# Kernel tuning notes

Measured on AMD Instinct MI355X. Metric: run time of the kernel, lower is better.

Reference implementation:

```python
import jax, jax.numpy as jnp
import numpy as np

B, T, C, H, E, TOPK, DR = 2, 2048, 768, 3072, 8, 2, 24


def setup_inputs() -> dict:
    key = jax.random.key(0)
    ks = jax.random.split(key, 16)
    std = 0.02
    n = lambda k, shape, s=std: (s * jax.random.normal(k, shape)).astype(jnp.float32)
    emb = jax.random.normal(ks[3], (E, DR), dtype=jnp.float32)
    emb = emb / (jnp.linalg.norm(emb, axis=-1, keepdims=True) + 1e-8)
    return {
        "x": jax.random.normal(ks[0], (B, T, C), dtype=jnp.float32),
        "router_w": n(ks[1], (E, C)),
        "probe_w": n(ks[2], (DR, C)),
        "router_emb": emb,
        "fatigue": jnp.zeros((E,), jnp.float32),
        "energy": jnp.ones((E,), jnp.float32),
        "w_fast1": n(ks[4], (E, C, H)),
        "w_slow1": n(ks[5], (E, C, H)),
        "h_fast1": n(ks[6], (E, C, H), 0.005),
        "m_gate1": jax.random.uniform(ks[7], (E,), dtype=jnp.float32),
        "b1": jnp.zeros((E, H), jnp.float32),
        "w_fast2": n(ks[8], (E, H, C)),
        "w_slow2": n(ks[9], (E, H, C)),
        "h_fast2": n(ks[10], (E, H, C), 0.005),
        "m_gate2": jax.random.uniform(ks[11], (E,), dtype=jnp.float32),
        "b2": jnp.zeros((E, C), jnp.float32),
    }


def _normalize(v, axis=-1, eps=1e-12):
    # matches F.normalize: v / max(||v||, eps)
    return v / jnp.maximum(jnp.linalg.norm(v, axis=axis, keepdims=True), eps)


def reference(x, router_w, probe_w, router_emb, fatigue, energy,
              w_fast1, w_slow1, h_fast1, m_gate1, b1,
              w_fast2, w_slow2, h_fast2, m_gate2, b2):
    Bd, Td, Cd = x.shape
    # --- router logits with biology-inspired biases ---
    logits = jnp.einsum('btc,ec->bte', x, router_w)            # nn.Linear, no bias
    tok_proxy = x.mean(axis=-1, keepdims=True)                  # [B,T,1]
    router_gain = jnp.linalg.norm(router_emb, axis=-1)          # [E]
    base_bias = 0.02 * tok_proxy                                # broadcasts over E
    gain_bias = 0.02 * tok_proxy * router_gain                  # [B,T,E]
    tok_unit = _normalize(jnp.einsum('btc,dc->btd', x, probe_w))
    align_bias = 0.02 * jnp.einsum('btd,ed->bte', tok_unit, _normalize(router_emb))
    logits = logits + base_bias + gain_bias + align_bias + 0.1 * energy - 0.1 * fatigue
    # --- top-k gating ---
    g, idx = jax.lax.top_k(logits, TOPK)                        # [B,T,K]
    gates = jax.nn.softmax(g, axis=-1)
    N = Bd * Td
    gates_full = jnp.zeros((N, E), x.dtype).at[
        jnp.arange(N)[:, None], idx.reshape(N, TOPK)].set(gates.reshape(N, TOPK))
    flat_x = x.reshape(N, Cd)
    # --- expert dispatch: dynamic W = w_fast + m_gate*w_slow + H_fast ---
    def body(acc, p):
        wf1, ws1, hf1, mg1, bb1, wf2, ws2, hf2, mg2, bb2, ge = p
        W1 = wf1 + mg1 * ws1 + hf1                              # [C,H]
        h = jnp.square(jnp.maximum(flat_x @ W1 + bb1, 0.0))     # relu(y)^2
        W2 = wf2 + mg2 * ws2 + hf2                              # [H,C]
        y = h @ W2 + bb2
        return acc + ge[:, None] * y, None
    out, _ = jax.lax.scan(
        body, jnp.zeros((N, Cd), x.dtype),
        (w_fast1, w_slow1, h_fast1, m_gate1, b1,
         w_fast2, w_slow2, h_fast2, m_gate2, b2, gates_full.T))
    return out.reshape(Bd, Td, Cd)
```

## Files before the change

kernel.cpp:

```cpp
#include <hip/hip_runtime.h>

typedef unsigned short u16;
typedef __attribute__((ext_vector_type(8))) short short8;
typedef __attribute__((ext_vector_type(8))) unsigned short ushort8;
typedef __attribute__((ext_vector_type(4))) unsigned short ushort4v;
typedef __attribute__((ext_vector_type(4))) float f32x4;

static constexpr int Cdim = 768;
static constexpr int Hdim = 3072;
static constexpr int Edim = 8;
static constexpr int Ntok = 4096;
static constexpr int DRc  = 24;
static constexpr int NSLOT = Ntok * 2;
static constexpr int NCHUNK = 8;
static constexpr int CCH = Cdim / NCHUNK;

static constexpr size_t OFF_XB   = 0;
static constexpr size_t OFF_W1T  = 6291456;
static constexpr size_t OFF_W2T  = 44040192;
static constexpr size_t OFF_HBUF = 81788928;
static constexpr size_t OFF_XT   = OFF_HBUF;
static constexpr size_t OFF_PART = OFF_HBUF + 12582912;
static constexpr size_t OFF_YB   = OFF_W1T;
static constexpr size_t OFF_TOK  = 132120576;
static constexpr size_t OFF_CNT  = 132382720;
static constexpr size_t OFF_OFFS = 132382752;
static constexpr size_t OFF_TSLOT= 132382784;
static constexpr size_t OFF_TG   = 132448320;

__device__ __forceinline__ u16 f2bf(float f) {
  unsigned u = __builtin_bit_cast(unsigned, f);
  u += 0x7fffu + ((u >> 16) & 1u);
  return (u16)(u >> 16);
}

__device__ __forceinline__ void gld16(const u16* g, u16* l) {
  __builtin_amdgcn_global_load_lds((const __attribute__((address_space(1))) unsigned int*)g,
                                   (__attribute__((address_space(3))) unsigned int*)l,
                                   16, 0, 0);
}

__global__ __launch_bounds__(256)
void prep_x2_kernel(const float* __restrict__ x, u16* __restrict__ x16,
                    float* __restrict__ xT) {
  __shared__ float tile[64][65];
  const int c0 = blockIdx.x * 64;
  const int t0 = blockIdx.y * 64;
  const int tid = threadIdx.x;
  const int row = tid >> 4, col = (tid & 15) * 4;
  #pragma unroll
  for (int i = 0; i < 4; i++) {
    int r = row + i * 16;
    size_t idx = (size_t)(t0 + r) * Cdim + c0 + col;
    float4 v = *(const float4*)(x + idx);
    tile[r][col + 0] = v.x; tile[r][col + 1] = v.y;
    tile[r][col + 2] = v.z; tile[r][col + 3] = v.w;
    ushort4v o = { f2bf(v.x), f2bf(v.y), f2bf(v.z), f2bf(v.w) };
    *reinterpret_cast<ushort4v*>(x16 + idx) = o;
  }
  __syncthreads();
  const int c = tid >> 2, tg = (tid & 3) * 16;
  #pragma unroll
  for (int q = 0; q < 4; q++) {
    float4 w;
    w.x = tile[tg + q * 4 + 0][c];
    w.y = tile[tg + q * 4 + 1][c];
    w.z = tile[tg + q * 4 + 2][c];
    w.w = tile[tg + q * 4 + 3][c];
    *reinterpret_cast<float4*>(xT + (size_t)(c0 + c) * Ntok + t0 + tg + q * 4) = w;
  }
}

__global__ __launch_bounds__(256)
void prep_wt_kernel(const float* __restrict__ wf, const float* __restrict__ wsl,
                    const float* __restrict__ hf, const float* __restrict__ mg,
                    u16* __restrict__ outw, const int R, const int Ccol) {
  __shared__ u16 tileT[64][66];
  const int e = blockIdx.z;
  const int r0 = blockIdx.x * 64, c0 = blockIdx.y * 64;
  const float m = mg[e];
  const size_t base = (size_t)e * R * Ccol;
  const int t = threadIdx.x;
  const int cr = t >> 4, cc = (t & 15) * 4;
  #pragma unroll
  for (int i = 0; i < 4; i++) {
    int r = cr + i * 16;
    size_t idx = base + (size_t)(r0 + r) * Ccol + (c0 + cc);
    float4 a = *(const float4*)(wf + idx);
    float4 b = *(const float4*)(wsl + idx);
    float4 h = *(const float4*)(hf + idx);
    tileT[cc + 0][r] = f2bf(fmaf(m, b.x, a.x) + h.x);
    tileT[cc + 1][r] = f2bf(fmaf(m, b.y, a.y) + h.y);
    tileT[cc + 2][r] = f2bf(fmaf(m, b.z, a.z) + h.z);
    tileT[cc + 3][r] = f2bf(fmaf(m, b.w, a.w) + h.w);
  }
  __syncthreads();
  const int oc = t >> 2, ch = (t & 3) * 16;
  ushort8 o0, o1;
  #pragma unroll
  for (int j = 0; j < 8; j++) { o0[j] = tileT[oc][ch + j]; o1[j] = tileT[oc][ch + 8 + j]; }
  size_t oidx = ((size_t)e * Ccol + c0 + oc) * R + r0 + ch;
  *reinterpret_cast<ushort8*>(outw + oidx) = o0;
  *reinterpret_cast<ushort8*>(outw + oidx + 8) = o1;
}

__global__ __launch_bounds__(256)
void logits_part_kernel(const float* __restrict__ xT, const float* __restrict__ router_w,
                        const float* __restrict__ probe_w, float* __restrict__ part) {
  const int t = blockIdx.x * 256 + threadIdx.x;
  const int cB = blockIdx.y * CCH;
  float racc[Edim] = {};
  float pacc[DRc] = {};
  float sacc = 0.f;
  for (int ci = 0; ci < CCH; ci++) {
    int c = cB + ci;
    float xv = xT[(size_t)c * Ntok + t];
    sacc += xv;
    #pragma unroll
    for (int ee = 0; ee < Edim; ee++) racc[ee] = fmaf(xv, router_w[ee * Cdim + c], racc[ee]);
    #pragma unroll
    for (int d = 0; d < DRc; d++) pacc[d] = fmaf(xv, probe_w[d * Cdim + c], pacc[d]);
  }
  float* pb = part + (size_t)blockIdx.y * 33 * Ntok + t;
  #pragma unroll
  for (int ee = 0; ee < Edim; ee++) pb[(size_t)ee * Ntok] = racc[ee];
  #pragma unroll
  for (int d = 0; d < DRc; d++) pb[(size_t)(8 + d) * Ntok] = pacc[d];
  pb[(size_t)32 * Ntok] = sacc;
}

__global__ __launch_bounds__(256)
void router_fin_kernel(const float* __restrict__ part, const float* __restrict__ emb,
                       const float* __restrict__ fatigue, const float* __restrict__ energy,
                       int* __restrict__ counts, int* __restrict__ tok_list,
                       int4* __restrict__ tokslot, float2* __restrict__ tokgate) {
  const int t = blockIdx.x * 256 + threadIdx.x;
  float v[33];
  #pragma unroll
  for (int o = 0; o < 33; o++) {
    float s = 0.f;
    #pragma unroll
    for (int ch = 0; ch < NCHUNK; ch++)
      s += part[((size_t)ch * 33 + o) * Ntok + t];
    v[o] = s;
  }
  const float* racc = v;
  const float* pacc = v + 8;
  float proxy = v[32] / 768.f;
  float pn2 = 0.f;
  #pragma unroll
  for (int d = 0; d < DRc; d++) pn2 += pacc[d] * pacc[d];
  float pnorm = sqrtf(pn2);
  float logitv[Edim];
  #pragma unroll
  for (int ee = 0; ee < Edim; ee++) {
    float g2 = 0.f, dote = 0.f;
    #pragma unroll
    for (int d = 0; d < DRc; d++) {
      float ev = emb[ee * DRc + d];
      g2 += ev * ev;
      dote += pacc[d] * ev;
    }
    float gain = sqrtf(g2);
    float align = dote / (fmaxf(pnorm, 1e-12f) * fmaxf(gain, 1e-12f));
    logitv[ee] = racc[ee] + 0.02f * proxy * (1.f + gain) + 0.02f * align
               + 0.1f * energy[ee] - 0.1f * fatigue[ee];
  }
  int e0 = 0; float b0v = logitv[0];
  #pragma unroll
  for (int ee = 1; ee < Edim; ee++) if (logitv[ee] > b0v) { b0v = logitv[ee]; e0 = ee; }
  int e1 = -1; float b1v = -3.4e38f;
  #pragma unroll
  for (int ee = 0; ee < Edim; ee++) if (ee != e0 && logitv[ee] > b1v) { b1v = logitv[ee]; e1 = ee; }
  float texp = expf(b1v - b0v);
  float g0 = 1.f / (1.f + texp);
  float g1 = texp / (1.f + texp);
  int p0 = atomicAdd(&counts[e0], 1);
  tok_list[e0 * Ntok + p0] = t;
  int p1 = atomicAdd(&counts[e1], 1);
  tok_list[e1 * Ntok + p1] = t;
  tokslot[t] = make_int4(e0, p0, e1, p1);
  tokgate[t] = make_float2(g0, g1);
}

__global__ void offsets_kernel(const int* __restrict__ counts, int* __restrict__ offs) {
  if (threadIdx.x == 0) {
    int r = 0;
    for (int e = 0; e < Edim; e++) { offs[e] = r; r += counts[e]; }
  }
}

__global__ __launch_bounds__(256)
void fc1_kernel(const u16* __restrict__ x16, const u16* __restrict__ W1T,
                const float* __restrict__ b1, const int* __restrict__ counts,
                const int* __restrict__ offs, const int* __restrict__ tok_list,
                u16* __restrict__ h_buf) {
  const int e = blockIdx.z;
  const int n_e = counts[e];
  const int tokBase = blockIdx.y * 128;
  if (tokBase >= n_e) return;
  const int hBase = blockIdx.x * 128;
  __shared__ u16 As[2][4096];
  __shared__ u16 Bs[2][4096];
  __shared__ int toks[128];
  const int tid = threadIdx.x;
  if (tid < 128) {
    int s = tokBase + tid;
    toks[tid] = (s < n_e) ? tok_list[e * Ntok + s] : 0;
  }
  __syncthreads();
  const int lane = tid & 63, wv = tid >> 6;
  const int wr = wv >> 1, wc = wv & 1;
  const int sRow = lane >> 2, sSlot = lane & 3;
  const int kbOff = (sSlot ^ ((sRow >> 1) & 3)) * 8;
  const int rA0 = wv * 16 + sRow, rA1 = 64 + rA0;
  const u16* pA0 = x16 + (size_t)toks[rA0] * Cdim + kbOff;
  const u16* pA1 = x16 + (size_t)toks[rA1] * Cdim + kbOff;
  const u16* pB0 = W1T + ((size_t)e * Hdim + hBase + rA0) * Cdim + kbOff;
  const u16* pB1 = W1T + ((size_t)e * Hdim + hBase + rA1) * Cdim + kbOff;
  const int stOff = wv * 512 + lane * 8;
  const int fr = lane & 15;
  const int qsw = (((lane >> 4) ^ ((fr >> 1) & 3))) * 8;
  f32x4 acc[4][4] = {};
  gld16(pA0, &As[0][stOff]);
  gld16(pA1, &As[0][2048 + stOff]);
  gld16(pB0, &Bs[0][stOff]);
  gld16(pB1, &Bs[0][2048 + stOff]);
  __syncthreads();
  int cur = 0;
  for (int it = 0; it < 24; it++) {
    if (it < 23) {
      int k1 = (it + 1) * 32;
      gld16(pA0 + k1, &As[cur ^ 1][stOff]);
      gld16(pA1 + k1, &As[cur ^ 1][2048 + stOff]);
      gld16(pB0 + k1, &Bs[cur ^ 1][stOff]);
      gld16(pB1 + k1, &Bs[cur ^ 1][2048 + stOff]);
    }
    short8 aF[4], bF[4];
    #pragma unroll
    for (int m = 0; m < 4; m++)
      aF[m] = *reinterpret_cast<const short8*>(&As[cur][(wr * 64 + m * 16 + fr) * 32 + qsw]);
    #pragma unroll
    for (int n = 0; n < 4; n++)
      bF[n] = *reinterpret_cast<const short8*>(&Bs[cur][(wc * 64 + n * 16 + fr) * 32 + qsw]);
    #pragma unroll
    for (int m = 0; m < 4; m++)
      #pragma unroll
      for (int n = 0; n < 4; n++)
        acc[m][n] = __builtin_amdgcn_mfma_f32_16x16x32_bf16(aF[m], bF[n], acc[m][n], 0, 0, 0);
    __syncthreads();
    cur ^= 1;
  }
  const int rq = (lane >> 4) * 4;
  float bias[4];
  #pragma unroll
  for (int n = 0; n < 4; n++) bias[n] = b1[(size_t)e * Hdim + hBase + wc * 64 + n * 16 + fr];
  const int rowB = offs[e] + tokBase;
  #pragma unroll
  for (int m = 0; m < 4; m++) {
    #pragma unroll
    for (int j = 0; j < 4; j++) {
      int rl = wr * 64 + m * 16 + rq + j;
      if (tokBase + rl < n_e) {
        size_t rb = (size_t)(rowB + rl) * Hdim + hBase + wc * 64 + fr;
        #pragma unroll
        for (int n = 0; n < 4; n++) {
          float v = fmaxf(acc[m][n][j] + bias[n], 0.f);
          h_buf[rb + n * 16] = f2bf(v * v);
        }
      }
    }
  }
}

__global__ __launch_bounds__(256)
void fc2_kernel(const u16* __restrict__ h_buf, const u16* __restrict__ W2T,
                const float* __restrict__ b2, const int* __restrict__ counts,
                const int* __restrict__ offs, float* __restrict__ ybuf) {
  const int e = blockIdx.z;
  const int n_e = counts[e];
  const int tokBase = blockIdx.y * 128;
  if (tokBase >= n_e) return;
  const int cBase = blockIdx.x * 128;
  __shared__ u16 As[2][4096];
  __shared__ u16 Bs[2][4096];
  const int tid = threadIdx.x;
  const int lane = tid & 63, wv = tid >> 6;
  const int wr = wv >> 1, wc = wv & 1;
  const int sRow = lane >> 2, sSlot = lane & 3;
  const int kbOff = (sSlot ^ ((sRow >> 1) & 3)) * 8;
  const int rA0 = wv * 16 + sRow, rA1 = 64 + rA0;
  const int slotB = offs[e] + tokBase;
  const int s0 = min(slotB + rA0, NSLOT - 1);
  const int s1 = min(slotB + rA1, NSLOT - 1);
  const u16* pA0 = h_buf + (size_t)s0 * Hdim + kbOff;
  const u16* pA1 = h_buf + (size_t)s1 * Hdim + kbOff;
  const u16* pB0 = W2T + ((size_t)e * Cdim + cBase + rA0) * Hdim + kbOff;
  const u16* pB1 = W2T + ((size_t)e * Cdim + cBase + rA1) * Hdim + kbOff;
  const int stOff = wv * 512 + lane * 8;
  const int fr = lane & 15;
  const int qsw = (((lane >> 4) ^ ((fr >> 1) & 3))) * 8;
  f32x4 acc[4][4] = {};
  gld16(pA0, &As[0][stOff]);
  gld16(pA1, &As[0][2048 + stOff]);
  gld16(pB0, &Bs[0][stOff]);
  gld16(pB1, &Bs[0][2048 + stOff]);
  __syncthreads();
  int cur = 0;
  for (int it = 0; it < 96; it++) {
    if (it < 95) {
      int k1 = (it + 1) * 32;
      gld16(pA0 + k1, &As[cur ^ 1][stOff]);
      gld16(pA1 + k1, &As[cur ^ 1][2048 + stOff]);
      gld16(pB0 + k1, &Bs[cur ^ 1][stOff]);
      gld16(pB1 + k1, &Bs[cur ^ 1][2048 + stOff]);
    }
    short8 aF[4], bF[4];
    #pragma unroll
    for (int m = 0; m < 4; m++)
      aF[m] = *reinterpret_cast<const short8*>(&As[cur][(wr * 64 + m * 16 + fr) * 32 + qsw]);
    #pragma unroll
    for (int n = 0; n < 4; n++)
      bF[n] = *reinterpret_cast<const short8*>(&Bs[cur][(wc * 64 + n * 16 + fr) * 32 + qsw]);
    #pragma unroll
    for (int m = 0; m < 4; m++)
      #pragma unroll
      for (int n = 0; n < 4; n++)
        acc[m][n] = __builtin_amdgcn_mfma_f32_16x16x32_bf16(aF[m], bF[n], acc[m][n], 0, 0, 0);
    __syncthreads();
    cur ^= 1;
  }
  const int rq = (lane >> 4) * 4;
  float bias[4];
  #pragma unroll
  for (int n = 0; n < 4; n++)
    bias[n] = b2[(size_t)e * Cdim + cBase + wc * 64 + n * 16 + fr];
  #pragma unroll
  for (int m = 0; m < 4; m++) {
    #pragma unroll
    for (int j = 0; j < 4; j++) {
      int rl = wr * 64 + m * 16 + rq + j;
      if (tokBase + rl < n_e) {
        float* ob = ybuf + (size_t)(slotB + rl) * Cdim + cBase + wc * 64 + fr;
        #pragma unroll
        for (int n = 0; n < 4; n++)
          ob[n * 16] = acc[m][n][j] + bias[n];
      }
    }
  }
}

__global__ __launch_bounds__(256)
void gather_kernel(const float* __restrict__ ybuf, const int4* __restrict__ tokslot,
                   const float2* __restrict__ tokgate, const int* __restrict__ offs,
                   float* __restrict__ out) {
  const int gid = blockIdx.x * 256 + threadIdx.x;
  const int t = gid / 192;
  const int c4 = (gid - t * 192) * 4;
  int4 ts = tokslot[t];
  float2 g = tokgate[t];
  int s0 = offs[ts.x] + ts.y;
  int s1 = offs[ts.z] + ts.w;
  float4 y0 = *reinterpret_cast<const float4*>(ybuf + (size_t)s0 * Cdim + c4);
  float4 y1 = *reinterpret_cast<const float4*>(ybuf + (size_t)s1 * Cdim + c4);
  float4 o;
  o.x = g.x * y0.x + g.y * y1.x;
  o.y = g.x * y0.y + g.y * y1.y;
  o.z = g.x * y0.z + g.y * y1.z;
  o.w = g.x * y0.w + g.y * y1.w;
  *reinterpret_cast<float4*>(out + (size_t)t * Cdim + c4) = o;
}

extern "C" void kernel_launch(void* const* d_in, const int* in_sizes, int n_in,
                              void* d_out, int out_size, void* d_ws, size_t ws_size,
                              hipStream_t stream) {
  const float* x        = (const float*)d_in[0];
  const float* router_w = (const float*)d_in[1];
  const float* probe_w  = (const float*)d_in[2];
  const float* emb      = (const float*)d_in[3];
  const float* fatigue  = (const float*)d_in[4];
  const float* energy   = (const float*)d_in[5];
  const float* wf1      = (const float*)d_in[6];
  const float* ws1      = (const float*)d_in[7];
  const float* hf1      = (const float*)d_in[8];
  const float* mg1      = (const float*)d_in[9];
  const float* b1       = (const float*)d_in[10];
  const float* wf2      = (const float*)d_in[11];
  const float* ws2      = (const float*)d_in[12];
  const float* hf2      = (const float*)d_in[13];
  const float* mg2      = (const float*)d_in[14];
  const float* b2       = (const float*)d_in[15];
  float* out = (float*)d_out;
  char* ws = (char*)d_ws;

  u16*    x16       = (u16*)(ws + OFF_XB);
  u16*    W1T       = (u16*)(ws + OFF_W1T);
  u16*    W2T       = (u16*)(ws + OFF_W2T);
  u16*    hbuf      = (u16*)(ws + OFF_HBUF);
  float*  xT        = (float*)(ws + OFF_XT);
  float*  part      = (float*)(ws + OFF_PART);
  float*  ybuf      = (float*)(ws + OFF_YB);
  int*    tok_list  = (int*)(ws + OFF_TOK);
  int*    counts    = (int*)(ws + OFF_CNT);
  int*    offs      = (int*)(ws + OFF_OFFS);
  int4*   tokslot   = (int4*)(ws + OFF_TSLOT);
  float2* tokgate   = (float2*)(ws + OFF_TG);

  hipMemsetAsync(counts, 0, 64, stream);

  prep_x2_kernel<<<dim3(Cdim / 64, Ntok / 64), 256, 0, stream>>>(x, x16, xT);
  logits_part_kernel<<<dim3(Ntok / 256, NCHUNK), 256, 0, stream>>>(xT, router_w, probe_w, part);
  router_fin_kernel<<<Ntok / 256, 256, 0, stream>>>(part, emb, fatigue, energy,
                                                    counts, tok_list, tokslot, tokgate);
  prep_wt_kernel<<<dim3(Cdim / 64, Hdim / 64, Edim), 256, 0, stream>>>(wf1, ws1, hf1, mg1, W1T, Cdim, Hdim);
  prep_wt_kernel<<<dim3(Hdim / 64, Cdim / 64, Edim), 256, 0, stream>>>(wf2, ws2, hf2, mg2, W2T, Hdim, Cdim);
  offsets_kernel<<<1, 64, 0, stream>>>(counts, offs);
  fc1_kernel<<<dim3(Hdim / 128, Ntok / 128, Edim), 256, 0, stream>>>(x16, W1T, b1, counts, offs,
                                                                     tok_list, hbuf);
  fc2_kernel<<<dim3(Cdim / 128, Ntok / 128, Edim), 256, 0, stream>>>(hbuf, W2T, b2, counts, offs,
                                                                     ybuf);
  gather_kernel<<<Ntok * 192 / 256, 256, 0, stream>>>(ybuf, tokslot, tokgate, offs, out);
  (void)in_sizes; (void)n_in; (void)out_size; (void)ws_size;
}
```

Before: 390.9 us.

## Split fc2 reduction dimension in two and store bf16 partials summed in gather

The fc2 GEMM now splits its H reduction into two halves, doubling the number of blocks, so more CUs are busy when per-expert token tiles are few. Each half writes a separate bf16 partial output buffer, with bias added only by the first half. The gather kernel loads both partials per slot and sums them before applying the gates. This costs extra partial-buffer traffic and adds bf16 rounding of the fc2 outputs, which lowers precision. The wider grid and halved per-block K loop are meant to reduce fc2 tail and under-occupancy costs.

Result: faster. 371.7 us (-4.9%).

```diff
diff --git a/kernel.cpp b/kernel.cpp
--- a/kernel.cpp
+++ b/kernel.cpp
@@ -14,6 +14,8 @@
 static constexpr int NSLOT = Ntok * 2;
 static constexpr int NCHUNK = 8;
 static constexpr int CCH = Cdim / NCHUNK;
+static constexpr int KS2 = 2;
+static constexpr int KC2 = Hdim / KS2;
 
 static constexpr size_t OFF_XB   = 0;
 static constexpr size_t OFF_W1T  = 6291456;
@@ -32,6 +34,11 @@
   unsigned u = __builtin_bit_cast(unsigned, f);
   u += 0x7fffu + ((u >> 16) & 1u);
   return (u16)(u >> 16);
+}
+
+__device__ __forceinline__ float bf2f(u16 v) {
+  unsigned u = ((unsigned)v) << 16;
+  return __builtin_bit_cast(float, u);
 }
 
 __device__ __forceinline__ void gld16(const u16* g, u16* l) {
@@ -276,12 +283,15 @@
 __global__ __launch_bounds__(256)
 void fc2_kernel(const u16* __restrict__ h_buf, const u16* __restrict__ W2T,
                 const float* __restrict__ b2, const int* __restrict__ counts,
-                const int* __restrict__ offs, float* __restrict__ ybuf) {
+                const int* __restrict__ offs, u16* __restrict__ ybuf) {
   const int e = blockIdx.z;
   const int n_e = counts[e];
   const int tokBase = blockIdx.y * 128;
   if (tokBase >= n_e) return;
-  const int cBase = blockIdx.x * 128;
+  const int xb = blockIdx.x;
+  const int kch = xb / 6;
+  const int cBase = (xb % 6) * 128;
+  const size_t kOff = (size_t)kch * KC2;
   __shared__ u16 As[2][4096];
   __shared__ u16 Bs[2][4096];
   const int tid = threadIdx.x;
@@ -293,10 +303,10 @@
   const int slotB = offs[e] + tokBase;
   const int s0 = min(slotB + rA0, NSLOT - 1);
   const int s1 = min(slotB + rA1, NSLOT - 1);
-  const u16* pA0 = h_buf + (size_t)s0 * Hdim + kbOff;
-  const u16* pA1 = h_buf + (size_t)s1 * Hdim + kbOff;
-  const u16* pB0 = W2T + ((size_t)e * Cdim + cBase + rA0) * Hdim + kbOff;
-  const u16* pB1 = W2T + ((size_t)e * Cdim + cBase + rA1) * Hdim + kbOff;
+  const u16* pA0 = h_buf + (size_t)s0 * Hdim + kOff + kbOff;
+  const u16* pA1 = h_buf + (size_t)s1 * Hdim + kOff + kbOff;
+  const u16* pB0 = W2T + ((size_t)e * Cdim + cBase + rA0) * Hdim + kOff + kbOff;
+  const u16* pB1 = W2T + ((size_t)e * Cdim + cBase + rA1) * Hdim + kOff + kbOff;
   const int stOff = wv * 512 + lane * 8;
   const int fr = lane & 15;
   const int qsw = (((lane >> 4) ^ ((fr >> 1) & 3))) * 8;
@@ -307,8 +317,8 @@
   gld16(pB1, &Bs[0][2048 + stOff]);
   __syncthreads();
   int cur = 0;
-  for (int it = 0; it < 96; it++) {
-    if (it < 95) {
+  for (int it = 0; it < 48; it++) {
+    if (it < 47) {
       int k1 = (it + 1) * 32;
       gld16(pA0 + k1, &As[cur ^ 1][stOff]);
       gld16(pA1 + k1, &As[cur ^ 1][2048 + stOff]);
@@ -334,24 +344,25 @@
   float bias[4];
   #pragma unroll
   for (int n = 0; n < 4; n++)
-    bias[n] = b2[(size_t)e * Cdim + cBase + wc * 64 + n * 16 + fr];
+    bias[n] = (kch == 0) ? b2[(size_t)e * Cdim + cBase + wc * 64 + n * 16 + fr] : 0.f;
+  u16* yb = ybuf + (size_t)kch * NSLOT * Cdim;
   #pragma unroll
   for (int m = 0; m < 4; m++) {
     #pragma unroll
     for (int j = 0; j < 4; j++) {
       int rl = wr * 64 + m * 16 + rq + j;
       if (tokBase + rl < n_e) {
-        float* ob = ybuf + (size_t)(slotB + rl) * Cdim + cBase + wc * 64 + fr;
+        u16* ob = yb + (size_t)(slotB + rl) * Cdim + cBase + wc * 64 + fr;
         #pragma unroll
         for (int n = 0; n < 4; n++)
-          ob[n * 16] = acc[m][n][j] + bias[n];
+          ob[n * 16] = f2bf(acc[m][n][j] + bias[n]);
       }
     }
   }
 }
 
 __global__ __launch_bounds__(256)
-void gather_kernel(const float* __restrict__ ybuf, const int4* __restrict__ tokslot,
+void gather_kernel(const u16* __restrict__ ybuf, const int4* __restrict__ tokslot,
                    const float2* __restrict__ tokgate, const int* __restrict__ offs,
                    float* __restrict__ out) {
   const int gid = blockIdx.x * 256 + threadIdx.x;
@@ -359,15 +370,18 @@
   const int c4 = (gid - t * 192) * 4;
   int4 ts = tokslot[t];
   float2 g = tokgate[t];
-  int s0 = offs[ts.x] + ts.y;
-  int s1 = offs[ts.z] + ts.w;
-  float4 y0 = *reinterpret_cast<const float4*>(ybuf + (size_t)s0 * Cdim + c4);
-  float4 y1 = *reinterpret_cast<const float4*>(ybuf + (size_t)s1 * Cdim + c4);
+  size_t s0 = (size_t)(offs[ts.x] + ts.y) * Cdim + c4;
+  size_t s1 = (size_t)(offs[ts.z] + ts.w) * Cdim + c4;
+  const size_t K1 = (size_t)NSLOT * Cdim;
+  ushort4v a0 = *reinterpret_cast<const ushort4v*>(ybuf + s0);
+  ushort4v a1 = *reinterpret_cast<const ushort4v*>(ybuf + K1 + s0);
+  ushort4v b0 = *reinterpret_cast<const ushort4v*>(ybuf + s1);
+  ushort4v b1 = *reinterpret_cast<const ushort4v*>(ybuf + K1 + s1);
   float4 o;
-  o.x = g.x * y0.x + g.y * y1.x;
-  o.y = g.x * y0.y + g.y * y1.y;
-  o.z = g.x * y0.z + g.y * y1.z;
-  o.w = g.x * y0.w + g.y * y1.w;
+  o.x = g.x * (bf2f(a0[0]) + bf2f(a1[0])) + g.y * (bf2f(b0[0]) + bf2f(b1[0]));
+  o.y = g.x * (bf2f(a0[1]) + bf2f(a1[1])) + g.y * (bf2f(b0[1]) + bf2f(b1[1]));
+  o.z = g.x * (bf2f(a0[2]) + bf2f(a1[2])) + g.y * (bf2f(b0[2]) + bf2f(b1[2]));
+  o.w = g.x * (bf2f(a0[3]) + bf2f(a1[3])) + g.y * (bf2f(b0[3]) + bf2f(b1[3]));
   *reinterpret_cast<float4*>(out + (size_t)t * Cdim + c4) = o;
 }
 
@@ -399,7 +413,7 @@
   u16*    hbuf      = (u16*)(ws + OFF_HBUF);
   float*  xT        = (float*)(ws + OFF_XT);
   float*  part      = (float*)(ws + OFF_PART);
-  float*  ybuf      = (float*)(ws + OFF_YB);
+  u16*    ybuf      = (u16*)(ws + OFF_YB);
   int*    tok_list  = (int*)(ws + OFF_TOK);
   int*    counts    = (int*)(ws + OFF_CNT);
   int*    offs      = (int*)(ws + OFF_OFFS);
@@ -417,8 +431,8 @@
   offsets_kernel<<<1, 64, 0, stream>>>(counts, offs);
   fc1_kernel<<<dim3(Hdim / 128, Ntok / 128, Edim), 256, 0, stream>>>(x16, W1T, b1, counts, offs,
                                                                      tok_list, hbuf);
-  fc2_kernel<<<dim3(Cdim / 128, Ntok / 128, Edim), 256, 0, stream>>>(hbuf, W2T, b2, counts, offs,
-                                                                     ybuf);
+  fc2_kernel<<<dim3(6 * KS2, Ntok / 128, Edim), 256, 0, stream>>>(hbuf, W2T, b2, counts, offs,
+                                                                  ybuf);
   gather_kernel<<<Ntok * 192 / 256, 256, 0, stream>>>(ybuf, tokslot, tokgate, offs, out);
   (void)in_sizes; (void)n_in; (void)out_size; (void)ws_size;
 }
```
